# Optimization experiments

Hardware: AMD Instinct MI355X
Metric: run time of the kernel (lower is better)

The kernel has to match this reference:

```python
import jax, jax.numpy as jnp
import numpy as np

# Config (matches init_kwargs)
B, DIM = 16, 768
HEADS, DHEAD = 12, 64
H_MEM, W_MEM = 16, 16           # memory grid; N = 256 tokens
MAX_AH, MAX_AW = 3, 3
N = H_MEM * W_MEM


def _area_pool(t):
    """t: [B', N, D] laid out on an H_MEM x W_MEM grid.
    Returns (area_sums [B', M, D], area_sizes [M]) over all rectangle sizes
    (ah, aw) with 1<=ah<=MAX_AH, 1<=aw<=MAX_AW, at every valid position,
    via a 2D integral image (summed-area table)."""
    Bp, _, D = t.shape
    g = t.reshape(Bp, H_MEM, W_MEM, D)
    I = jnp.cumsum(jnp.cumsum(g, axis=1), axis=2)
    I = jnp.pad(I, ((0, 0), (1, 0), (1, 0), (0, 0)))  # [B', H+1, W+1, D]
    sums, sizes = [], []
    for ah in range(1, MAX_AH + 1):
        for aw in range(1, MAX_AW + 1):
            s = (I[:, ah:, aw:] - I[:, :-ah, aw:]
                 - I[:, ah:, :-aw] + I[:, :-ah, :-aw])  # [B', H-ah+1, W-aw+1, D]
            n_pos = s.shape[1] * s.shape[2]
            sums.append(s.reshape(Bp, n_pos, D))
            sizes.append(np.full((n_pos,), float(ah * aw), dtype=np.float32))
    return jnp.concatenate(sums, axis=1), jnp.asarray(np.concatenate(sizes))


def setup_inputs() -> dict:
    key = jax.random.key(0)
    ks = jax.random.split(key, 10)
    s = 0.02
    d = dict(
        x=jax.random.normal(ks[0], (B, N, DIM), jnp.float32),
        # to_qkv: Linear(dim, 3*dim, bias=False); stored as (in, out)
        w_qkv=jax.random.normal(ks[1], (DIM, 3 * DIM), jnp.float32) * s,
        # per-head q/k/v projections (dim -> heads*dim_head) with bias
        w_q=jax.random.normal(ks[2], (DIM, HEADS * DHEAD), jnp.float32) * s,
        b_q=jnp.zeros((HEADS * DHEAD,), jnp.float32),
        w_k=jax.random.normal(ks[3], (DIM, HEADS * DHEAD), jnp.float32) * s,
        b_k=jnp.zeros((HEADS * DHEAD,), jnp.float32),
        w_v=jax.random.normal(ks[4], (DIM, HEADS * DHEAD), jnp.float32) * s,
        b_v=jnp.zeros((HEADS * DHEAD,), jnp.float32),
        # output projection (heads*dim_head -> dim)
        w_o=jax.random.normal(ks[5], (HEADS * DHEAD, DIM), jnp.float32) * s,
        b_o=jnp.zeros((DIM,), jnp.float32),
    )
    return d


def reference(x, w_qkv, w_q, b_q, w_k, b_k, w_v, b_v, w_o, b_o):
    # QKV projection + split: 'b n (qkv d) -> qkv b n d'
    qkv = x @ w_qkv                               # [B, N, 3*DIM]
    q, k, v = jnp.split(qkv, 3, axis=-1)          # each [B, N, DIM]

    def to_heads(t, w, b):                        # 'b n (h d) -> (b h) n d'
        return ((t @ w + b)
                .reshape(B, N, HEADS, DHEAD)
                .transpose(0, 2, 1, 3)
                .reshape(B * HEADS, N, DHEAD))

    qh = to_heads(q, w_q, b_q)
    kh = to_heads(k, w_k, b_k)
    vh = to_heads(v, w_v, b_v)

    # Area keys: mean over each area; area values: sum over each area.
    k_sum, sizes = _area_pool(kh)                 # [BH, M, d], [M]
    k_area = k_sum / sizes[None, :, None]
    v_area, _ = _area_pool(vh)                    # [BH, M, d]

    logits = jnp.einsum('bqd,bmd->bqm', qh, k_area)   # [BH, N, M]
    weights = jax.nn.softmax(logits, axis=-1)
    out = jnp.einsum('bqm,bmd->bqd', weights, v_area)  # [BH, N, d]

    # '(b h) n d -> b n (h d)' then output projection
    out = (out.reshape(B, HEADS, N, DHEAD)
              .transpose(0, 2, 1, 3)
              .reshape(B, N, HEADS * DHEAD))
    return out @ w_o + b_o
```

## Files before the change

### kernel.cpp

```cpp
#include <hip/hip_runtime.h>
#include <hip/hip_bf16.h>

typedef __hip_bfloat16 bf16;
typedef __attribute__((ext_vector_type(8))) short short8b;
typedef __attribute__((ext_vector_type(4))) short short4b;
typedef __attribute__((ext_vector_type(4))) float f32x4;

#define NAREA 2025
#define NAREA_PAD 2048

static __device__ __forceinline__ float b2f(bf16 x) { return __bfloat162float(x); }
static __device__ __forceinline__ short f2bs(float f) {
  bf16 h = __float2bfloat16(f);
  return *(short*)&h;
}

__global__ __launch_bounds__(256) void k_prep(
    const float* __restrict__ x, const float* __restrict__ wqkv,
    const float* __restrict__ wq, const float* __restrict__ wk,
    const float* __restrict__ wv,
    bf16* __restrict__ xb, bf16* __restrict__ wqkvb,
    bf16* __restrict__ wqT, bf16* __restrict__ wkT, bf16* __restrict__ wvT,
    int4* __restrict__ rectG, float* __restrict__ invG)
{
  __shared__ float tile[32][33];
  int b = blockIdx.x;
  if (b < 4800) {
    int idx = (b * 256 + threadIdx.x) * 4;
    const int NX = 4096 * 768;
    float4 v;
    bf16* d;
    if (idx < NX) { v = *(const float4*)(x + idx); d = xb + idx; }
    else { v = *(const float4*)(wqkv + (idx - NX)); d = wqkvb + (idx - NX); }
    short4b s = {f2bs(v.x), f2bs(v.y), f2bs(v.z), f2bs(v.w)};
    *(short4b*)d = s;
    return;
  }
  if (b < 6528) {
    int r = b - 4800;
    int z = r / 576; r -= z * 576;
    int by = r / 24, bx = r - by * 24;
    const float* src = (z == 0) ? wq : (z == 1) ? wk : wv;
    bf16* dst = (z == 0) ? wqT : (z == 1) ? wkT : wvT;
    int r0 = by * 32, c0 = bx * 32;
    int lx = threadIdx.x & 31, ly = threadIdx.x >> 5;
#pragma unroll
    for (int yy = 0; yy < 4; ++yy)
      tile[ly + yy * 8][lx] = src[(size_t)(r0 + ly + yy * 8) * 768 + c0 + lx];
    __syncthreads();
#pragma unroll
    for (int yy = 0; yy < 4; ++yy)
      dst[(size_t)(c0 + ly + yy * 8) * 768 + r0 + lx] =
          __float2bfloat16(tile[lx][ly + yy * 8]);
    return;
  }
  int m = (b - 6528) * 256 + threadIdx.x;
  if (m >= NAREA_PAD) return;
  int4 rc = make_int4(0, 0, 0, 0);
  float iv = 0.f;
  if (m < NAREA) {
    int rem = m, ah = 1, aw = 1, found = 0;
    for (int a = 1; a <= 3 && !found; ++a)
      for (int w = 1; w <= 3 && !found; ++w) {
        int np = (17 - a) * (17 - w);
        if (rem < np) { ah = a; aw = w; found = 1; }
        else rem -= np;
      }
    int cw = 17 - aw;
    int y = rem / cw, xx = rem - y * cw;
    rc.x = (y * 17 + xx) * 64;
    rc.y = (y * 17 + (xx + aw)) * 64;
    rc.z = ((y + ah) * 17 + xx) * 64;
    rc.w = ((y + ah) * 17 + (xx + aw)) * 64;
    iv = 1.0f / (float)(ah * aw);
  }
  rectG[m] = rc;
  invG[m] = iv;
}

__global__ __launch_bounds__(256) void k_tcast1(
    const float* __restrict__ src, bf16* __restrict__ dst)
{
  __shared__ float tile[32][33];
  int r0 = blockIdx.y * 32, c0 = blockIdx.x * 32;
  int lx = threadIdx.x & 31, ly = threadIdx.x >> 5;
#pragma unroll
  for (int yy = 0; yy < 4; ++yy)
    tile[ly + yy * 8][lx] = src[(size_t)(r0 + ly + yy * 8) * 768 + c0 + lx];
  __syncthreads();
#pragma unroll
  for (int yy = 0; yy < 4; ++yy)
    dst[(size_t)(c0 + ly + yy * 8) * 768 + r0 + lx] =
        __float2bfloat16(tile[lx][ly + yy * 8]);
}


__global__ __launch_bounds__(256) void k_combine_m(
    const bf16* __restrict__ wqkvb, const bf16* __restrict__ wqT,
    const bf16* __restrict__ wkT, const bf16* __restrict__ wvT,
    bf16* __restrict__ WcTb)
{
  __shared__ __align__(16) short As[2][128 * 32];
  __shared__ __align__(16) short Bs[2][128 * 32];
  const int t3 = blockIdx.z;
  const bf16* BT = (t3 == 0) ? wqT : (t3 == 1) ? wkT : wvT;
  const int m0 = blockIdx.y * 128, n0 = blockIdx.x * 128;
  const int tid = threadIdx.x, lane = tid & 63, w = tid >> 6;
  const int tt = lane & 15, q4 = lane >> 4;
  const int moff = (w & 1) * 64, noff = (w >> 1) * 64;
  const int r_a = tid >> 2, kc = (tid & 3) * 8;

  f32x4 acc[4][4];
#pragma unroll
  for (int i = 0; i < 4; ++i)
#pragma unroll
    for (int j = 0; j < 4; ++j) acc[i][j] = (f32x4){0.f, 0.f, 0.f, 0.f};

  uint4 ra0 = *(const uint4*)(wqkvb + (size_t)(m0 + r_a) * 2304 + t3 * 768 + kc);
  uint4 ra1 = *(const uint4*)(wqkvb + (size_t)(m0 + r_a + 64) * 2304 + t3 * 768 + kc);
  uint4 rb0 = *(const uint4*)(BT + (size_t)(n0 + r_a) * 768 + kc);
  uint4 rb1 = *(const uint4*)(BT + (size_t)(n0 + r_a + 64) * 768 + kc);

  for (int it = 0; it < 24; ++it) {
    short* as = As[it & 1];
    short* bs = Bs[it & 1];
    *(uint4*)&as[r_a * 32 + kc] = ra0;
    *(uint4*)&as[(r_a + 64) * 32 + kc] = ra1;
    *(uint4*)&bs[r_a * 32 + kc] = rb0;
    *(uint4*)&bs[(r_a + 64) * 32 + kc] = rb1;
    if (it < 23) {
      int k0 = (it + 1) * 32;
      ra0 = *(const uint4*)(wqkvb + (size_t)(m0 + r_a) * 2304 + t3 * 768 + k0 + kc);
      ra1 = *(const uint4*)(wqkvb + (size_t)(m0 + r_a + 64) * 2304 + t3 * 768 + k0 + kc);
      rb0 = *(const uint4*)(BT + (size_t)(n0 + r_a) * 768 + k0 + kc);
      rb1 = *(const uint4*)(BT + (size_t)(n0 + r_a + 64) * 768 + k0 + kc);
    }
    __syncthreads();
    short8b afr[4], bfr[4];
#pragma unroll
    for (int mt = 0; mt < 4; ++mt)
      afr[mt] = *(const short8b*)&as[(moff + mt * 16 + tt) * 32 + q4 * 8];
#pragma unroll
    for (int nt = 0; nt < 4; ++nt)
      bfr[nt] = *(const short8b*)&bs[(noff + nt * 16 + tt) * 32 + q4 * 8];
#pragma unroll
    for (int mt = 0; mt < 4; ++mt)
#pragma unroll
      for (int nt = 0; nt < 4; ++nt)
        acc[mt][nt] = __builtin_amdgcn_mfma_f32_16x16x32_bf16(afr[mt], bfr[nt], acc[mt][nt], 0, 0, 0);
  }

  bf16* C = WcTb + (size_t)t3 * 768 * 768;
#pragma unroll
  for (int nt = 0; nt < 4; ++nt) {
    int n = n0 + noff + nt * 16 + tt;
#pragma unroll
    for (int mt = 0; mt < 4; ++mt) {
      int mb = m0 + moff + mt * 16 + q4 * 4;
      short4b v = {f2bs(acc[mt][nt][0]), f2bs(acc[mt][nt][1]),
                   f2bs(acc[mt][nt][2]), f2bs(acc[mt][nt][3])};
      *(short4b*)&C[(size_t)n * 768 + mb] = v;
    }
  }
}

__global__ __launch_bounds__(256) void k_proj_m(
    const bf16* __restrict__ xb, const bf16* __restrict__ WcTb,
    const float* __restrict__ bq, const float* __restrict__ bk,
    const float* __restrict__ bv,
    bf16* __restrict__ qh, bf16* __restrict__ kh, bf16* __restrict__ vh)
{
  __shared__ __align__(16) short As[2][128 * 32];
  __shared__ __align__(16) short Bs[2][128 * 32];
  const int t3 = blockIdx.z;
  const bf16* BT = WcTb + (size_t)t3 * 768 * 768;
  const float* bias = (t3 == 0) ? bq : (t3 == 1) ? bk : bv;
  bf16* dst = (t3 == 0) ? qh : (t3 == 1) ? kh : vh;
  const int m0 = blockIdx.y * 128, n0 = blockIdx.x * 128;
  const int tid = threadIdx.x, lane = tid & 63, w = tid >> 6;
  const int tt = lane & 15, q4 = lane >> 4;
  const int moff = (w & 1) * 64, noff = (w >> 1) * 64;
  const int r_a = tid >> 2, kc = (tid & 3) * 8;

  f32x4 acc[4][4];
#pragma unroll
  for (int i = 0; i < 4; ++i)
#pragma unroll
    for (int j = 0; j < 4; ++j) acc[i][j] = (f32x4){0.f, 0.f, 0.f, 0.f};

  uint4 ra0 = *(const uint4*)(xb + (size_t)(m0 + r_a) * 768 + kc);
  uint4 ra1 = *(const uint4*)(xb + (size_t)(m0 + r_a + 64) * 768 + kc);
  uint4 rb0 = *(const uint4*)(BT + (size_t)(n0 + r_a) * 768 + kc);
  uint4 rb1 = *(const uint4*)(BT + (size_t)(n0 + r_a + 64) * 768 + kc);

  for (int it = 0; it < 24; ++it) {
    short* as = As[it & 1];
    short* bs = Bs[it & 1];
    *(uint4*)&as[r_a * 32 + kc] = ra0;
    *(uint4*)&as[(r_a + 64) * 32 + kc] = ra1;
    *(uint4*)&bs[r_a * 32 + kc] = rb0;
    *(uint4*)&bs[(r_a + 64) * 32 + kc] = rb1;
    if (it < 23) {
      int k0 = (it + 1) * 32;
      ra0 = *(const uint4*)(xb + (size_t)(m0 + r_a) * 768 + k0 + kc);
      ra1 = *(const uint4*)(xb + (size_t)(m0 + r_a + 64) * 768 + k0 + kc);
      rb0 = *(const uint4*)(BT + (size_t)(n0 + r_a) * 768 + k0 + kc);
      rb1 = *(const uint4*)(BT + (size_t)(n0 + r_a + 64) * 768 + k0 + kc);
    }
    __syncthreads();
    short8b afr[4], bfr[4];
#pragma unroll
    for (int mt = 0; mt < 4; ++mt)
      afr[mt] = *(const short8b*)&as[(moff + mt * 16 + tt) * 32 + q4 * 8];
#pragma unroll
    for (int nt = 0; nt < 4; ++nt)
      bfr[nt] = *(const short8b*)&bs[(noff + nt * 16 + tt) * 32 + q4 * 8];
#pragma unroll
    for (int mt = 0; mt < 4; ++mt)
#pragma unroll
      for (int nt = 0; nt < 4; ++nt)
        acc[mt][nt] = __builtin_amdgcn_mfma_f32_16x16x32_bf16(afr[mt], bfr[nt], acc[mt][nt], 0, 0, 0);
  }

#pragma unroll
  for (int nt = 0; nt < 4; ++nt) {
    int c = n0 + noff + nt * 16 + tt;
    float bvv = bias[c];
    int h = c >> 6, d = c & 63;
#pragma unroll
    for (int mt = 0; mt < 4; ++mt) {
#pragma unroll
      for (int r = 0; r < 4; ++r) {
        int m = m0 + moff + mt * 16 + q4 * 4 + r;
        dst[(((size_t)((m >> 8) * 12 + h)) << 14) + ((m & 255) << 6) + d] =
            __float2bfloat16(acc[mt][nt][r] + bvv);
      }
    }
  }
}

__global__ __launch_bounds__(256) void k_out_m(
    const bf16* __restrict__ attno, const bf16* __restrict__ woT,
    const float* __restrict__ bo, float* __restrict__ out)
{
  __shared__ __align__(16) short As[2][128 * 32];
  __shared__ __align__(16) short Bs[2][128 * 32];
  const int m0 = blockIdx.y * 128, n0 = blockIdx.x * 128;
  const int tid = threadIdx.x, lane = tid & 63, w = tid >> 6;
  const int tt = lane & 15, q4 = lane >> 4;
  const int moff = (w & 1) * 64, noff = (w >> 1) * 64;
  const int r_a = tid >> 2, kc = (tid & 3) * 8;

  f32x4 acc[4][4];
#pragma unroll
  for (int i = 0; i < 4; ++i)
#pragma unroll
    for (int j = 0; j < 4; ++j) acc[i][j] = (f32x4){0.f, 0.f, 0.f, 0.f};

  int m_a0 = m0 + r_a, m_a1 = m0 + r_a + 64;
  uint4 ra0 = *(const uint4*)(attno + (((size_t)((m_a0 >> 8) * 12 + (kc >> 6))) << 14) + ((m_a0 & 255) << 6) + (kc & 63));
  uint4 ra1 = *(const uint4*)(attno + (((size_t)((m_a1 >> 8) * 12 + (kc >> 6))) << 14) + ((m_a1 & 255) << 6) + (kc & 63));
  uint4 rb0 = *(const uint4*)(woT + (size_t)(n0 + r_a) * 768 + kc);
  uint4 rb1 = *(const uint4*)(woT + (size_t)(n0 + r_a + 64) * 768 + kc);

  for (int it = 0; it < 24; ++it) {
    short* as = As[it & 1];
    short* bs = Bs[it & 1];
    *(uint4*)&as[r_a * 32 + kc] = ra0;
    *(uint4*)&as[(r_a + 64) * 32 + kc] = ra1;
    *(uint4*)&bs[r_a * 32 + kc] = rb0;
    *(uint4*)&bs[(r_a + 64) * 32 + kc] = rb1;
    if (it < 23) {
      int k = (it + 1) * 32 + kc;
      ra0 = *(const uint4*)(attno + (((size_t)((m_a0 >> 8) * 12 + (k >> 6))) << 14) + ((m_a0 & 255) << 6) + (k & 63));
      ra1 = *(const uint4*)(attno + (((size_t)((m_a1 >> 8) * 12 + (k >> 6))) << 14) + ((m_a1 & 255) << 6) + (k & 63));
      rb0 = *(const uint4*)(woT + (size_t)(n0 + r_a) * 768 + k);
      rb1 = *(const uint4*)(woT + (size_t)(n0 + r_a + 64) * 768 + k);
    }
    __syncthreads();
    short8b afr[4], bfr[4];
#pragma unroll
    for (int mt = 0; mt < 4; ++mt)
      afr[mt] = *(const short8b*)&as[(moff + mt * 16 + tt) * 32 + q4 * 8];
#pragma unroll
    for (int nt = 0; nt < 4; ++nt)
      bfr[nt] = *(const short8b*)&bs[(noff + nt * 16 + tt) * 32 + q4 * 8];
#pragma unroll
    for (int mt = 0; mt < 4; ++mt)
#pragma unroll
      for (int nt = 0; nt < 4; ++nt)
        acc[mt][nt] = __builtin_amdgcn_mfma_f32_16x16x32_bf16(afr[mt], bfr[nt], acc[mt][nt], 0, 0, 0);
  }

#pragma unroll
  for (int nt = 0; nt < 4; ++nt) {
    int c = n0 + noff + nt * 16 + tt;
    float bvv = bo[c];
#pragma unroll
    for (int mt = 0; mt < 4; ++mt)
#pragma unroll
      for (int r = 0; r < 4; ++r) {
        int m = m0 + moff + mt * 16 + q4 * 4 + r;
        out[(size_t)m * 768 + c] = acc[mt][nt][r] + bvv;
      }
  }
}

__global__ __launch_bounds__(1024) void k_integral_p(
    const bf16* __restrict__ kh, const bf16* __restrict__ vh,
    float* __restrict__ Ik, float* __restrict__ Iv)
{
  __shared__ float sat[17 * 17 * 64];
  int bh = blockIdx.x >> 1;
  bool isv = blockIdx.x & 1;
  const bf16* src = (isv ? vh : kh) + ((size_t)bh << 14);
  float* dst = (isv ? Iv : Ik) + (size_t)bh * 18496;
  int tid = threadIdx.x;
  int d = tid & 63;
  int row = tid >> 6;
  {
    float run = 0.f;
    sat[((row + 1) * 17) * 64 + d] = 0.f;
#pragma unroll
    for (int xx = 0; xx < 16; ++xx) {
      run += b2f(src[(row * 16 + xx) * 64 + d]);
      sat[((row + 1) * 17 + (xx + 1)) * 64 + d] = run;
    }
    if (row == 0) {
#pragma unroll
      for (int xx = 0; xx < 17; ++xx) sat[xx * 64 + d] = 0.f;
    }
  }
  __syncthreads();
  {
    int x = row + 1;
    float run = 0.f;
#pragma unroll
    for (int y = 1; y <= 16; ++y) {
      run += sat[(y * 17 + x) * 64 + d];
      sat[(y * 17 + x) * 64 + d] = run;
    }
  }
  __syncthreads();
  for (int i = tid; i < 18496; i += 1024) dst[i] = sat[i];
}

__global__ __launch_bounds__(1024) void k_attn_m(
    const bf16* __restrict__ qh, const float* __restrict__ Ik,
    const float* __restrict__ Iv, const int4* __restrict__ rectG,
    const float* __restrict__ invG, bf16* __restrict__ attno)
{
  __shared__ __align__(16) short aK2[2][64 * 72];
  __shared__ __align__(16) short aVt2[2][64 * 72];
  __shared__ __align__(16) short Pb[16][16 * 72];

  const int tid = threadIdx.x;
  const int lane = tid & 63;
  const int w = tid >> 6;
  const int t = lane & 15;
  const int q4 = lane >> 4;
  const int bh = blockIdx.x;

  const float* Ikb = Ik + (size_t)bh * 18496;
  const float* Ivb = Iv + (size_t)bh * 18496;
  const bf16* qbase = qh + ((size_t)bh << 14);

  short8b qf0 = *(const short8b*)(qbase + (w * 16 + t) * 64 + q4 * 8);
  short8b qf1 = *(const short8b*)(qbase + (w * 16 + t) * 64 + 32 + q4 * 8);

  f32x4 O[4];
#pragma unroll
  for (int i = 0; i < 4; ++i) O[i] = (f32x4){0.f, 0.f, 0.f, 0.f};
  float l = 0.f;

  {
    short* aK = aK2[0];
    short* aVt = aVt2[0];
    short vp[4];
#pragma unroll
    for (int i = 0; i < 4; ++i) {
      int j = w * 4 + i;
      int4 rc = rectG[j];
      float iv = invG[j];
      float kc = Ikb[rc.w + lane] - Ikb[rc.y + lane] - Ikb[rc.z + lane] + Ikb[rc.x + lane];
      float vc = Ivb[rc.w + lane] - Ivb[rc.y + lane] - Ivb[rc.z + lane] + Ivb[rc.x + lane];
      aK[j * 72 + lane] = f2bs(kc * iv);
      vp[i] = f2bs(vc);
    }
    *(short4b*)&aVt[lane * 72 + w * 4] = (short4b){vp[0], vp[1], vp[2], vp[3]};
  }

  float kcr[4], vcr[4], ivr[4];
  for (int it = 0; it < 32; ++it) {
    if (it + 1 < 32) {
      int t0n = (it + 1) * 64;
#pragma unroll
      for (int i = 0; i < 4; ++i) {
        int j = t0n + w * 4 + i;
        int4 rc = rectG[j];
        ivr[i] = invG[j];
        kcr[i] = Ikb[rc.w + lane] - Ikb[rc.y + lane] - Ikb[rc.z + lane] + Ikb[rc.x + lane];
        vcr[i] = Ivb[rc.w + lane] - Ivb[rc.y + lane] - Ivb[rc.z + lane] + Ivb[rc.x + lane];
      }
    }
    __syncthreads();
    const short* aK = aK2[it & 1];
    const short* aVt = aVt2[it & 1];
    if (it + 1 < 32) {
      short* aKn = aK2[(it + 1) & 1];
      short* aVtn = aVt2[(it + 1) & 1];
      short vp[4];
#pragma unroll
      for (int i = 0; i < 4; ++i) {
        aKn[(w * 4 + i) * 72 + lane] = f2bs(kcr[i] * ivr[i]);
        vp[i] = f2bs(vcr[i]);
      }
      *(short4b*)&aVtn[lane * 72 + w * 4] = (short4b){vp[0], vp[1], vp[2], vp[3]};
    }

    const int t0 = it * 64;
    const bool edge = (t0 + 64 > NAREA);
#pragma unroll
    for (int at = 0; at < 4; ++at) {
      short8b af0 = *(const short8b*)&aK[(at * 16 + t) * 72 + q4 * 8];
      short8b af1 = *(const short8b*)&aK[(at * 16 + t) * 72 + 32 + q4 * 8];
      f32x4 s = (f32x4){0.f, 0.f, 0.f, 0.f};
      s = __builtin_amdgcn_mfma_f32_16x16x32_bf16(af0, qf0, s, 0, 0, 0);
      s = __builtin_amdgcn_mfma_f32_16x16x32_bf16(af1, qf1, s, 0, 0, 0);
      float p[4];
#pragma unroll
      for (int r = 0; r < 4; ++r) {
        p[r] = __expf(s[r]);
        if (edge && (t0 + at * 16 + q4 * 4 + r >= NAREA)) p[r] = 0.f;
      }
      l += (p[0] + p[1]) + (p[2] + p[3]);
      short4b pk = (short4b){f2bs(p[0]), f2bs(p[1]), f2bs(p[2]), f2bs(p[3])};
      *(short4b*)&Pb[w][t * 72 + at * 16 + q4 * 4] = pk;
    }
    short8b pf0 = *(const short8b*)&Pb[w][t * 72 + q4 * 8];
    short8b pf1 = *(const short8b*)&Pb[w][t * 72 + 32 + q4 * 8];
#pragma unroll
    for (int nt = 0; nt < 4; ++nt) {
      short8b vf0 = *(const short8b*)&aVt[(nt * 16 + t) * 72 + q4 * 8];
      short8b vf1 = *(const short8b*)&aVt[(nt * 16 + t) * 72 + 32 + q4 * 8];
      O[nt] = __builtin_amdgcn_mfma_f32_16x16x32_bf16(pf0, vf0, O[nt], 0, 0, 0);
      O[nt] = __builtin_amdgcn_mfma_f32_16x16x32_bf16(pf1, vf1, O[nt], 0, 0, 0);
    }
  }

  l += __shfl_xor(l, 16, 64);
  l += __shfl_xor(l, 32, 64);

  bf16* ob = attno + ((size_t)bh << 14);
#pragma unroll
  for (int r = 0; r < 4; ++r) {
    int qrow = q4 * 4 + r;
    float invl = 1.0f / __shfl(l, qrow, 64);
#pragma unroll
    for (int nt = 0; nt < 4; ++nt)
      ob[(w * 16 + qrow) * 64 + nt * 16 + t] = __float2bfloat16(O[nt][r] * invl);
  }
}

extern "C" void kernel_launch(void* const* d_in, const int* in_sizes, int n_in,
                              void* d_out, int out_size, void* d_ws, size_t ws_size,
                              hipStream_t stream) {
  const float* x    = (const float*)d_in[0];
  const float* wqkv = (const float*)d_in[1];
  const float* wq   = (const float*)d_in[2];
  const float* bq   = (const float*)d_in[3];
  const float* wk   = (const float*)d_in[4];
  const float* bk   = (const float*)d_in[5];
  const float* wv   = (const float*)d_in[6];
  const float* bv   = (const float*)d_in[7];
  const float* wo   = (const float*)d_in[8];
  const float* bo   = (const float*)d_in[9];
  float* out = (float*)d_out;

  char* ws = (char*)d_ws;
  char* ob = (char*)d_out;
  const size_t WC_B = 7077888;
  const size_t QH_B = 6291456;

  bf16* xb    = (bf16*)ob;
  bf16* WcTb  = (bf16*)(ob + QH_B);
  bf16* attno = (bf16*)ws;
  int4*  rectG = (int4*)(ws + QH_B);
  float* invG  = (float*)(ws + QH_B + 32768);
  bf16* qh = (bf16*)(ws + WC_B);
  bf16* kh = (bf16*)(ws + WC_B + QH_B);
  bf16* vh = (bf16*)(ws + WC_B + 2 * QH_B);
  bf16* wqkvb = (bf16*)(ws + WC_B);
  bf16* wqT   = (bf16*)(ws + WC_B + 3538944);
  bf16* wkT   = (bf16*)(ws + WC_B + 4718592);
  bf16* wvT   = (bf16*)(ws + WC_B + 5898240);
  float* Ik = (float*)(ws + WC_B + 3 * QH_B);
  float* Iv = Ik + 3551232;
  bf16* woT = (bf16*)(ws + WC_B + 3 * QH_B);

  k_prep<<<dim3(6536), 256, 0, stream>>>(x, wqkv, wq, wk, wv, xb, wqkvb,
                                         wqT, wkT, wvT, rectG, invG);
  k_combine_m<<<dim3(6, 6, 3), 256, 0, stream>>>(wqkvb, wqT, wkT, wvT, WcTb);
  k_proj_m<<<dim3(6, 32, 3), 256, 0, stream>>>(xb, WcTb, bq, bk, bv, qh, kh, vh);
  k_integral_p<<<dim3(384), 1024, 0, stream>>>(kh, vh, Ik, Iv);
  k_attn_m<<<dim3(192), 1024, 0, stream>>>(qh, Ik, Iv, rectG, invG, attno);
  k_tcast1<<<dim3(24, 24), 256, 0, stream>>>(wo, woT);
  k_out_m<<<dim3(6, 32), 256, 0, stream>>>(attno, woT, bo, out);
}
```

Baseline: 242.7 us.

## Use direct global-to-LDS loads in GEMMs and keep attention probabilities in registers

```diff
diff --git a/kernel.cpp b/kernel.cpp
--- a/kernel.cpp
+++ b/kernel.cpp
@@ -13,6 +13,13 @@
 static __device__ __forceinline__ short f2bs(float f) {
   bf16 h = __float2bfloat16(f);
   return *(short*)&h;
+}
+
+static __device__ __forceinline__ void gll16(const void* g, void* l) {
+  __builtin_amdgcn_global_load_lds(
+      (const __attribute__((address_space(1))) unsigned int*)(unsigned long long)g,
+      (__attribute__((address_space(3))) unsigned int*)(unsigned int)(unsigned long long)l,
+      16, 0, 0);
 }
 
 __global__ __launch_bounds__(256) void k_prep(
@@ -116,26 +123,23 @@
 #pragma unroll
     for (int j = 0; j < 4; ++j) acc[i][j] = (f32x4){0.f, 0.f, 0.f, 0.f};
 
-  uint4 ra0 = *(const uint4*)(wqkvb + (size_t)(m0 + r_a) * 2304 + t3 * 768 + kc);
-  uint4 ra1 = *(const uint4*)(wqkvb + (size_t)(m0 + r_a + 64) * 2304 + t3 * 768 + kc);
-  uint4 rb0 = *(const uint4*)(BT + (size_t)(n0 + r_a) * 768 + kc);
-  uint4 rb1 = *(const uint4*)(BT + (size_t)(n0 + r_a + 64) * 768 + kc);
-
+#define STAGE_C(k0, buf)                                                        \
+  {                                                                             \
+    gll16(wqkvb + (size_t)(m0 + r_a) * 2304 + t3 * 768 + (k0) + kc,             \
+          &As[buf][w * 512]);                                                   \
+    gll16(wqkvb + (size_t)(m0 + r_a + 64) * 2304 + t3 * 768 + (k0) + kc,        \
+          &As[buf][2048 + w * 512]);                                            \
+    gll16(BT + (size_t)(n0 + r_a) * 768 + (k0) + kc, &Bs[buf][w * 512]);        \
+    gll16(BT + (size_t)(n0 + r_a + 64) * 768 + (k0) + kc,                       \
+          &Bs[buf][2048 + w * 512]);                                            \
+  }
+
+  STAGE_C(0, 0);
   for (int it = 0; it < 24; ++it) {
-    short* as = As[it & 1];
-    short* bs = Bs[it & 1];
-    *(uint4*)&as[r_a * 32 + kc] = ra0;
-    *(uint4*)&as[(r_a + 64) * 32 + kc] = ra1;
-    *(uint4*)&bs[r_a * 32 + kc] = rb0;
-    *(uint4*)&bs[(r_a + 64) * 32 + kc] = rb1;
-    if (it < 23) {
-      int k0 = (it + 1) * 32;
-      ra0 = *(const uint4*)(wqkvb + (size_t)(m0 + r_a) * 2304 + t3 * 768 + k0 + kc);
-      ra1 = *(const uint4*)(wqkvb + (size_t)(m0 + r_a + 64) * 2304 + t3 * 768 + k0 + kc);
-      rb0 = *(const uint4*)(BT + (size_t)(n0 + r_a) * 768 + k0 + kc);
-      rb1 = *(const uint4*)(BT + (size_t)(n0 + r_a + 64) * 768 + k0 + kc);
-    }
     __syncthreads();
+    if (it < 23) STAGE_C((it + 1) * 32, (it + 1) & 1);
+    const short* as = As[it & 1];
+    const short* bs = Bs[it & 1];
     short8b afr[4], bfr[4];
 #pragma unroll
     for (int mt = 0; mt < 4; ++mt)
@@ -149,6 +153,7 @@
       for (int nt = 0; nt < 4; ++nt)
         acc[mt][nt] = __builtin_amdgcn_mfma_f32_16x16x32_bf16(afr[mt], bfr[nt], acc[mt][nt], 0, 0, 0);
   }
+#undef STAGE_C
 
   bf16* C = WcTb + (size_t)t3 * 768 * 768;
 #pragma unroll
@@ -188,26 +193,22 @@
 #pragma unroll
     for (int j = 0; j < 4; ++j) acc[i][j] = (f32x4){0.f, 0.f, 0.f, 0.f};
 
-  uint4 ra0 = *(const uint4*)(xb + (size_t)(m0 + r_a) * 768 + kc);
-  uint4 ra1 = *(const uint4*)(xb + (size_t)(m0 + r_a + 64) * 768 + kc);
-  uint4 rb0 = *(const uint4*)(BT + (size_t)(n0 + r_a) * 768 + kc);
-  uint4 rb1 = *(const uint4*)(BT + (size_t)(n0 + r_a + 64) * 768 + kc);
-
+#define STAGE_P(k0, buf)                                                        \
+  {                                                                             \
+    gll16(xb + (size_t)(m0 + r_a) * 768 + (k0) + kc, &As[buf][w * 512]);        \
+    gll16(xb + (size_t)(m0 + r_a + 64) * 768 + (k0) + kc,                       \
+          &As[buf][2048 + w * 512]);                                            \
+    gll16(BT + (size_t)(n0 + r_a) * 768 + (k0) + kc, &Bs[buf][w * 512]);        \
+    gll16(BT + (size_t)(n0 + r_a + 64) * 768 + (k0) + kc,                       \
+          &Bs[buf][2048 + w * 512]);                                            \
+  }
+
+  STAGE_P(0, 0);
   for (int it = 0; it < 24; ++it) {
-    short* as = As[it & 1];
-    short* bs = Bs[it & 1];
-    *(uint4*)&as[r_a * 32 + kc] = ra0;
-    *(uint4*)&as[(r_a + 64) * 32 + kc] = ra1;
-    *(uint4*)&bs[r_a * 32 + kc] = rb0;
-    *(uint4*)&bs[(r_a + 64) * 32 + kc] = rb1;
-    if (it < 23) {
-      int k0 = (it + 1) * 32;
-      ra0 = *(const uint4*)(xb + (size_t)(m0 + r_a) * 768 + k0 + kc);
-      ra1 = *(const uint4*)(xb + (size_t)(m0 + r_a + 64) * 768 + k0 + kc);
-      rb0 = *(const uint4*)(BT + (size_t)(n0 + r_a) * 768 + k0 + kc);
-      rb1 = *(const uint4*)(BT + (size_t)(n0 + r_a + 64) * 768 + k0 + kc);
-    }
     __syncthreads();
+    if (it < 23) STAGE_P((it + 1) * 32, (it + 1) & 1);
+    const short* as = As[it & 1];
+    const short* bs = Bs[it & 1];
     short8b afr[4], bfr[4];
 #pragma unroll
     for (int mt = 0; mt < 4; ++mt)
@@ -221,6 +222,7 @@
       for (int nt = 0; nt < 4; ++nt)
         acc[mt][nt] = __builtin_amdgcn_mfma_f32_16x16x32_bf16(afr[mt], bfr[nt], acc[mt][nt], 0, 0, 0);
   }
+#undef STAGE_P
 
 #pragma unroll
   for (int nt = 0; nt < 4; ++nt) {
@@ -250,6 +252,7 @@
   const int tt = lane & 15, q4 = lane >> 4;
   const int moff = (w & 1) * 64, noff = (w >> 1) * 64;
   const int r_a = tid >> 2, kc = (tid & 3) * 8;
+  const int m_a0 = m0 + r_a, m_a1 = m0 + r_a + 64;
 
   f32x4 acc[4][4];
 #pragma unroll
@@ -257,27 +260,25 @@
 #pragma unroll
     for (int j = 0; j < 4; ++j) acc[i][j] = (f32x4){0.f, 0.f, 0.f, 0.f};
 
-  int m_a0 = m0 + r_a, m_a1 = m0 + r_a + 64;
-  uint4 ra0 = *(const uint4*)(attno + (((size_t)((m_a0 >> 8) * 12 + (kc >> 6))) << 14) + ((m_a0 & 255) << 6) + (kc & 63));
-  uint4 ra1 = *(const uint4*)(attno + (((size_t)((m_a1 >> 8) * 12 + (kc >> 6))) << 14) + ((m_a1 & 255) << 6) + (kc & 63));
-  uint4 rb0 = *(const uint4*)(woT + (size_t)(n0 + r_a) * 768 + kc);
-  uint4 rb1 = *(const uint4*)(woT + (size_t)(n0 + r_a + 64) * 768 + kc);
-
+#define STAGE_O(k0, buf)                                                        \
+  {                                                                             \
+    int k = (k0) + kc;                                                          \
+    gll16(attno + (((size_t)((m_a0 >> 8) * 12 + (k >> 6))) << 14) +             \
+              ((m_a0 & 255) << 6) + (k & 63),                                   \
+          &As[buf][w * 512]);                                                   \
+    gll16(attno + (((size_t)((m_a1 >> 8) * 12 + (k >> 6))) << 14) +             \
+              ((m_a1 & 255) << 6) + (k & 63),                                   \
+          &As[buf][2048 + w * 512]);                                            \
+    gll16(woT + (size_t)(n0 + r_a) * 768 + k, &Bs[buf][w * 512]);               \
+    gll16(woT + (size_t)(n0 + r_a + 64) * 768 + k, &Bs[buf][2048 + w * 512]);   \
+  }
+
+  STAGE_O(0, 0);
   for (int it = 0; it < 24; ++it) {
-    short* as = As[it & 1];
-    short* bs = Bs[it & 1];
-    *(uint4*)&as[r_a * 32 + kc] = ra0;
-    *(uint4*)&as[(r_a + 64) * 32 + kc] = ra1;
-    *(uint4*)&bs[r_a * 32 + kc] = rb0;
-    *(uint4*)&bs[(r_a + 64) * 32 + kc] = rb1;
-    if (it < 23) {
-      int k = (it + 1) * 32 + kc;
-      ra0 = *(const uint4*)(attno + (((size_t)((m_a0 >> 8) * 12 + (k >> 6))) << 14) + ((m_a0 & 255) << 6) + (k & 63));
-      ra1 = *(const uint4*)(attno + (((size_t)((m_a1 >> 8) * 12 + (k >> 6))) << 14) + ((m_a1 & 255) << 6) + (k & 63));
-      rb0 = *(const uint4*)(woT + (size_t)(n0 + r_a) * 768 + k);
-      rb1 = *(const uint4*)(woT + (size_t)(n0 + r_a + 64) * 768 + k);
-    }
     __syncthreads();
+    if (it < 23) STAGE_O((it + 1) * 32, (it + 1) & 1);
+    const short* as = As[it & 1];
+    const short* bs = Bs[it & 1];
     short8b afr[4], bfr[4];
 #pragma unroll
     for (int mt = 0; mt < 4; ++mt)
@@ -291,6 +292,7 @@
       for (int nt = 0; nt < 4; ++nt)
         acc[mt][nt] = __builtin_amdgcn_mfma_f32_16x16x32_bf16(afr[mt], bfr[nt], acc[mt][nt], 0, 0, 0);
   }
+#undef STAGE_O
 
 #pragma unroll
   for (int nt = 0; nt < 4; ++nt) {
@@ -350,9 +352,8 @@
     const float* __restrict__ Iv, const int4* __restrict__ rectG,
     const float* __restrict__ invG, bf16* __restrict__ attno)
 {
-  __shared__ __align__(16) short aK2[2][64 * 72];
+  __shared__ __align__(16) short aK2[2][64 * 80];
   __shared__ __align__(16) short aVt2[2][64 * 72];
-  __shared__ __align__(16) short Pb[16][16 * 72];
 
   const int tid = threadIdx.x;
   const int lane = tid & 63;
@@ -360,6 +361,7 @@
   const int t = lane & 15;
   const int q4 = lane >> 4;
   const int bh = blockIdx.x;
+  const int rbase = (t & 12) * 2 + (t & 3);
 
   const float* Ikb = Ik + (size_t)bh * 18496;
   const float* Ivb = Iv + (size_t)bh * 18496;
@@ -384,7 +386,7 @@
       float iv = invG[j];
       float kc = Ikb[rc.w + lane] - Ikb[rc.y + lane] - Ikb[rc.z + lane] + Ikb[rc.x + lane];
       float vc = Ivb[rc.w + lane] - Ivb[rc.y + lane] - Ivb[rc.z + lane] + Ivb[rc.x + lane];
-      aK[j * 72 + lane] = f2bs(kc * iv);
+      aK[j * 80 + lane] = f2bs(kc * iv);
       vp[i] = f2bs(vc);
     }
     *(short4b*)&aVt[lane * 72 + w * 4] = (short4b){vp[0], vp[1], vp[2], vp[3]};
@@ -412,7 +414,7 @@
       short vp[4];
 #pragma unroll
       for (int i = 0; i < 4; ++i) {
-        aKn[(w * 4 + i) * 72 + lane] = f2bs(kcr[i] * ivr[i]);
+        aKn[(w * 4 + i) * 80 + lane] = f2bs(kcr[i] * ivr[i]);
         vp[i] = f2bs(vcr[i]);
       }
       *(short4b*)&aVtn[lane * 72 + w * 4] = (short4b){vp[0], vp[1], vp[2], vp[3]};
@@ -420,31 +422,36 @@
 
     const int t0 = it * 64;
     const bool edge = (t0 + 64 > NAREA);
+    union { short8b v; unsigned u[4]; } apv[2];
 #pragma unroll
     for (int at = 0; at < 4; ++at) {
-      short8b af0 = *(const short8b*)&aK[(at * 16 + t) * 72 + q4 * 8];
-      short8b af1 = *(const short8b*)&aK[(at * 16 + t) * 72 + 32 + q4 * 8];
+      int row = rbase + (at & 1) * 4 + (at >> 1) * 32;
+      short8b af0 = *(const short8b*)&aK[row * 80 + q4 * 8];
+      short8b af1 = *(const short8b*)&aK[row * 80 + 32 + q4 * 8];
       f32x4 s = (f32x4){0.f, 0.f, 0.f, 0.f};
       s = __builtin_amdgcn_mfma_f32_16x16x32_bf16(af0, qf0, s, 0, 0, 0);
       s = __builtin_amdgcn_mfma_f32_16x16x32_bf16(af1, qf1, s, 0, 0, 0);
+      int abase = t0 + (at >> 1) * 32 + q4 * 8 + (at & 1) * 4;
       float p[4];
 #pragma unroll
       for (int r = 0; r < 4; ++r) {
         p[r] = __expf(s[r]);
-        if (edge && (t0 + at * 16 + q4 * 4 + r >= NAREA)) p[r] = 0.f;
+        if (edge && (abase + r >= NAREA)) p[r] = 0.f;
       }
       l += (p[0] + p[1]) + (p[2] + p[3]);
-      short4b pk = (short4b){f2bs(p[0]), f2bs(p[1]), f2bs(p[2]), f2bs(p[3])};
-      *(short4b*)&Pb[w][t * 72 + at * 16 + q4 * 4] = pk;
-    }
-    short8b pf0 = *(const short8b*)&Pb[w][t * 72 + q4 * 8];
-    short8b pf1 = *(const short8b*)&Pb[w][t * 72 + 32 + q4 * 8];
+      unsigned lo = ((unsigned)(unsigned short)f2bs(p[1]) << 16) |
+                    (unsigned short)f2bs(p[0]);
+      unsigned hi = ((unsigned)(unsigned short)f2bs(p[3]) << 16) |
+                    (unsigned short)f2bs(p[2]);
+      apv[at >> 1].u[(at & 1) * 2 + 0] = lo;
+      apv[at >> 1].u[(at & 1) * 2 + 1] = hi;
+    }
 #pragma unroll
     for (int nt = 0; nt < 4; ++nt) {
       short8b vf0 = *(const short8b*)&aVt[(nt * 16 + t) * 72 + q4 * 8];
       short8b vf1 = *(const short8b*)&aVt[(nt * 16 + t) * 72 + 32 + q4 * 8];
-      O[nt] = __builtin_amdgcn_mfma_f32_16x16x32_bf16(pf0, vf0, O[nt], 0, 0, 0);
-      O[nt] = __builtin_amdgcn_mfma_f32_16x16x32_bf16(pf1, vf1, O[nt], 0, 0, 0);
+      O[nt] = __builtin_amdgcn_mfma_f32_16x16x32_bf16(apv[0].v, vf0, O[nt], 0, 0, 0);
+      O[nt] = __builtin_amdgcn_mfma_f32_16x16x32_bf16(apv[1].v, vf1, O[nt], 0, 0, 0);
     }
   }
 
```

After: 240.5 us. No clear change (-0.9%).
